# Optimization experiments

Measured on AMD Instinct MI355X. Metric: run time of the kernel, lower is better.

Reference implementation:

```python
import jax, jax.numpy as jnp
import numpy as np

BS, D_IN, D_H, D_Z = 4096, 784, 400, 20


def setup_inputs() -> dict:
    key = jax.random.key(0)
    ks = jax.random.split(key, 13)
    s = 0.05
    return {
        "x": jax.random.normal(ks[0], (BS, D_IN), dtype=jnp.float32),
        "W1": jax.random.normal(ks[1], (D_H, D_IN), dtype=jnp.float32) * s,
        "b1": jax.random.normal(ks[2], (D_H,), dtype=jnp.float32) * s,
        "W21": jax.random.normal(ks[3], (D_Z, D_H), dtype=jnp.float32) * s,
        "b21": jax.random.normal(ks[4], (D_Z,), dtype=jnp.float32) * s,
        "W22": jax.random.normal(ks[5], (D_Z, D_H), dtype=jnp.float32) * s,
        "b22": jax.random.normal(ks[6], (D_Z,), dtype=jnp.float32) * s,
        "W3": jax.random.normal(ks[7], (D_H, D_Z), dtype=jnp.float32) * s,
        "b3": jax.random.normal(ks[8], (D_H,), dtype=jnp.float32) * s,
        "W41": jax.random.normal(ks[9], (D_IN, D_H), dtype=jnp.float32) * s,
        "b41": jax.random.normal(ks[10], (D_IN,), dtype=jnp.float32) * s,
        "W42": jax.random.normal(ks[11], (D_IN, D_H), dtype=jnp.float32) * s,
        "b42": jax.random.normal(ks[12], (D_IN,), dtype=jnp.float32) * s,
    }


def reference(x, W1, b1, W21, b21, W22, b22, W3, b3, W41, b41, W42, b42):
    xr = x.reshape(-1, D_IN)                              # [bs, 784]
    # encode
    h1 = jax.nn.relu(xr @ W1.T + b1)                      # [bs, 400]
    mu = h1 @ W21.T + b21                                 # [bs, 20]
    logvar = h1 @ W22.T + b22                             # [bs, 20]
    # unscented sigma points: varsqrt[:, i] = sqrt(N)*logvar[:, i]*e_i
    N = D_Z
    sqrtN = jnp.asarray(np.sqrt(N), dtype=x.dtype)
    # delta[i, b, j] = sqrt(N) * logvar[b, i] * (i == j)   -> [N, bs, N]
    delta = sqrtN * logvar.T[:, :, None] * jnp.eye(N, dtype=x.dtype)[:, None, :]
    z = jnp.concatenate([mu[None] + delta, mu[None] - delta], axis=0)  # [2N, bs, N]

    def decode(zs):
        h3 = jax.nn.relu(zs @ W3.T + b3)                  # [bs, 400]
        return zs @ W41.T * 0 + (h3 @ W41.T + b41), h3 @ W42.T + b42

    def decode_clean(zs):
        h3 = jax.nn.relu(zs @ W3.T + b3)
        return h3 @ W41.T + b41, h3 @ W42.T + b42

    # original loop decodes every sigma point; recon_x keeps the last one
    mu_x, var_x = jax.vmap(decode_clean)(z)               # each [2N, bs, 784]
    recon_mu = mu_x[-1]
    recon_var = var_x[-1]
    return recon_mu, recon_var, mu, logvar, z
```

## Files before the change

### kernel.cpp

```cpp
#include <hip/hip_runtime.h>
#include <hip/hip_bf16.h>

#define BS   4096
#define DIN  784
#define DH   400
#define DZ   20

#define KPH  416
#define KPD  448

#define OFF_RMU  0
#define OFF_RVAR 3211264
#define OFF_MU   6422528
#define OFF_LV   6504448
#define OFF_Z    6586368

#define WS_WCAT  0
#define WS_W2C   1404928
#define WS_H1B   1444864
#define WS_H3B   4852736

#define SQRT20F 4.47213595499958f

using short8 = __attribute__((ext_vector_type(8))) short;
using f4     = __attribute__((ext_vector_type(4))) float;
using i4     = __attribute__((ext_vector_type(4))) int;

__device__ __forceinline__ short bf16r(float f) {
    union { float f; unsigned u; } v; v.f = f;
    unsigned r = (v.u + 0x7fffu + ((v.u >> 16) & 1u)) >> 16;
    return (short)r;
}

__device__ __forceinline__ i4 pack8(const i4 q0, const i4 q1) {
    i4 d;
    d[0] = (q0[1] & 0xffff0000) | (int)(((unsigned)q0[0]) >> 16);
    d[1] = (q0[3] & 0xffff0000) | (int)(((unsigned)q0[2]) >> 16);
    d[2] = (q1[1] & 0xffff0000) | (int)(((unsigned)q1[0]) >> 16);
    d[3] = (q1[3] & 0xffff0000) | (int)(((unsigned)q1[2]) >> 16);
    return d;
}

__device__ __forceinline__ void glds16(const void* g, void* l) {
    __builtin_amdgcn_global_load_lds(
        (const __attribute__((address_space(1))) unsigned int*)g,
        (__attribute__((address_space(3))) unsigned int*)l,
        16, 0, 0);
}

__global__ __launch_bounds__(256)
void k1(const float* __restrict__ x, const float* __restrict__ W1,
        const float* __restrict__ b1,
        const float* __restrict__ W41, const float* __restrict__ W42,
        const float* __restrict__ W21, const float* __restrict__ W22,
        short* __restrict__ h1b, char* __restrict__ ws) {
    __shared__ short sA[2][64 * 64];
    __shared__ short sB[2][80 * 64];

    const int tid = threadIdx.x;
    const int bid = blockIdx.x;

    if (bid >= 320) {
        short* wcat = (short*)(ws + WS_WCAT);
        short* w2c  = (short*)(ws + WS_W2C);
        const int NC = 1568 * 56 + 48 * 52;
        for (int p = (bid - 320) * 256 + tid; p < NC; p += 64 * 256) {
            const float* sr = nullptr;
            short* dst;
            int c;
            if (p < 1568 * 56) {
                int row = p / 56; c = p - row * 56;
                sr = (row < 784) ? (W41 + (size_t)row * DH)
                                 : (W42 + (size_t)(row - 784) * DH);
                dst = wcat + (size_t)row * KPD + c * 8;
            } else {
                int q = p - 1568 * 56;
                int row = q / 52; c = q - row * 52;
                if (row < 20)      sr = W21 + (size_t)row * DH;
                else if (row < 40) sr = W22 + (size_t)(row - 20) * DH;
                dst = w2c + (size_t)row * KPH + c * 8;
            }
            short8 v;
            if (c < 50 && sr) {
                f4 a = *(const f4*)(sr + c * 8);
                f4 b = *(const f4*)(sr + c * 8 + 4);
#pragma unroll
                for (int e = 0; e < 4; ++e) { v[e] = bf16r(a[e]); v[4 + e] = bf16r(b[e]); }
            } else {
#pragma unroll
                for (int e = 0; e < 8; ++e) v[e] = 0;
            }
            *(short8*)dst = v;
        }
        return;
    }

    const int swz = (bid & 7) * 40 + (bid >> 3);
    const int bm = swz / 5, bn = swz - bm * 5;
    const int w = tid >> 6, l = tid & 63, lg = l >> 4, lr = l & 15;

    f4 acc[5] = {};
    i4 A0[4], A1[4], B0[6], B1[6];

    auto loadT = [&](int kt, i4* qa, i4* qb) {
#pragma unroll
        for (int i = 0; i < 2; ++i) {
            int c = tid + i * 256;
            int row = c >> 3, kc = c & 7;
            int gk = kt * 64 + kc * 8;
            if (gk < DIN) {
                const i4* p = (const i4*)(x + (size_t)(bm * 64 + row) * DIN + gk);
                qa[2 * i] = p[0]; qa[2 * i + 1] = p[1];
            } else {
                qa[2 * i] = (i4){0, 0, 0, 0}; qa[2 * i + 1] = (i4){0, 0, 0, 0};
            }
        }
#pragma unroll
        for (int i = 0; i < 3; ++i) {
            int c = tid + i * 256;
            if (c < 640) {
                int row = c >> 3, kc = c & 7;
                int gk = kt * 64 + kc * 8;
                if (gk < DIN) {
                    const i4* p = (const i4*)(W1 + (size_t)(bn * 80 + row) * DIN + gk);
                    qb[2 * i] = p[0]; qb[2 * i + 1] = p[1];
                } else {
                    qb[2 * i] = (i4){0, 0, 0, 0}; qb[2 * i + 1] = (i4){0, 0, 0, 0};
                }
            }
        }
    };
    auto writeT = [&](int buf, const i4* qa, const i4* qb) {
#pragma unroll
        for (int i = 0; i < 2; ++i) {
            int c = tid + i * 256;
            int row = c >> 3, kc = c & 7;
            *(i4*)&sA[buf][(row * 8 + (kc ^ (row & 7))) * 8] = pack8(qa[2 * i], qa[2 * i + 1]);
        }
#pragma unroll
        for (int i = 0; i < 3; ++i) {
            int c = tid + i * 256;
            if (c < 640) {
                int row = c >> 3, kc = c & 7;
                *(i4*)&sB[buf][(row * 8 + (kc ^ (row & 7))) * 8] = pack8(qb[2 * i], qb[2 * i + 1]);
            }
        }
    };
    auto compute = [&](int buf) {
        const int row = w * 16 + lr;
#pragma unroll
        for (int kk = 0; kk < 2; ++kk) {
            short8 a = *(const short8*)&sA[buf][(row * 8 + ((kk * 4 + lg) ^ (row & 7))) * 8];
#pragma unroll
            for (int ni = 0; ni < 5; ++ni) {
                int brw = ni * 16 + lr;
                short8 b = *(const short8*)&sB[buf][(brw * 8 + ((kk * 4 + lg) ^ (brw & 7))) * 8];
                acc[ni] = __builtin_amdgcn_mfma_f32_16x16x32_bf16(a, b, acc[ni], 0, 0, 0);
            }
        }
    };

    loadT(0, A0, B0);
    writeT(0, A0, B0);
    loadT(1, A1, B1);
    loadT(2, A0, B0);
    asm volatile("s_waitcnt lgkmcnt(0)" ::: "memory");
    __builtin_amdgcn_sched_barrier(0);
    __builtin_amdgcn_s_barrier();
    __builtin_amdgcn_sched_barrier(0);

#pragma unroll
    for (int kt2 = 0; kt2 < 13; kt2 += 2) {
        {
            const int kt = kt2;
            compute(0);
            if (kt <= 11) writeT(1, A1, B1);
            if (kt <= 9)  loadT(kt + 3, A1, B1);
            asm volatile("s_waitcnt lgkmcnt(0)" ::: "memory");
            __builtin_amdgcn_sched_barrier(0);
            __builtin_amdgcn_s_barrier();
            __builtin_amdgcn_sched_barrier(0);
        }
        if (kt2 + 1 < 13) {
            const int kt = kt2 + 1;
            compute(1);
            if (kt <= 11) writeT(0, A0, B0);
            if (kt <= 9)  loadT(kt + 3, A0, B0);
            asm volatile("s_waitcnt lgkmcnt(0)" ::: "memory");
            __builtin_amdgcn_sched_barrier(0);
            __builtin_amdgcn_s_barrier();
            __builtin_amdgcn_sched_barrier(0);
        }
    }

#pragma unroll
    for (int ni = 0; ni < 5; ++ni) {
        int col = bn * 80 + ni * 16 + lr;
        float bias = b1[col];
#pragma unroll
        for (int r = 0; r < 4; ++r) {
            int row = bm * 64 + w * 16 + lg * 4 + r;
            float v = acc[ni][r] + bias;
            h1b[(size_t)row * KPH + col] = bf16r(v > 0.f ? v : 0.f);
        }
    }
    if (bn == 4) {
        for (int p = tid; p < 64 * 16; p += 256) {
            int r = p >> 4, c = 400 + (p & 15);
            h1b[(size_t)(bm * 64 + r) * KPH + c] = 0;
        }
    }
}

__global__ __launch_bounds__(256)
void k_mid(const short* __restrict__ h1b, const short* __restrict__ w2c,
           const float* __restrict__ W3, const float* __restrict__ b3,
           const float* __restrict__ b21, const float* __restrict__ b22,
           float* __restrict__ out, short* __restrict__ h3b) {
    __shared__ short sA[16 * 416];
    __shared__ short sB[48 * 416];
    __shared__ short sW[400 * 40];
    __shared__ float muv[2][16][20];
    __shared__ short zl[16 * 40];
    __shared__ short h3s[16 * 448];

    const int tid = threadIdx.x;
    const int blk = blockIdx.x;
    const int w = tid >> 6, l = tid & 63, lg = l >> 4, lr = l & 15;
    const int r0 = blk * 16;

#pragma unroll
    for (int it = 0; it < 4; ++it) {
        int p = it * 256 + tid;
        if (p < 832) {
            int r = p / 52, cp = p - r * 52, c = cp ^ (r & 3);
            glds16(h1b + (size_t)(r0 + r) * KPH + c * 8, &sA[p * 8]);
        }
    }
#pragma unroll
    for (int it = 0; it < 10; ++it) {
        int p = it * 256 + tid;
        if (p < 2496) {
            int r = p / 52, cp = p - r * 52, c = cp ^ (r & 3);
            glds16(w2c + (size_t)r * KPH + c * 8, &sB[p * 8]);
        }
    }
    if (tid < 200) {
#pragma unroll
        for (int i = 0; i < 2; ++i) {
            int r = tid + i * 200;
            const float* src = W3 + (size_t)r * DZ;
            f4 f0 = *(const f4*)src;
            f4 f1 = *(const f4*)(src + 4);
            f4 f2 = *(const f4*)(src + 8);
            f4 f3 = *(const f4*)(src + 12);
            f4 f5 = *(const f4*)(src + 16);
            short8 c0, c1, c2, c3;
#pragma unroll
            for (int e = 0; e < 4; ++e) {
                c0[e] = bf16r(f0[e]); c0[4 + e] = bf16r(f1[e]);
                c1[e] = bf16r(f2[e]); c1[4 + e] = bf16r(f3[e]);
                c2[e] = bf16r(f5[e]); c2[4 + e] = 0;
                c3[e] = 0; c3[4 + e] = 0;
            }
            *(short8*)&sW[r * 40 + 0]  = c0;
            *(short8*)&sW[r * 40 + 8]  = c1;
            *(short8*)&sW[r * 40 + 16] = c2;
            *(short8*)&sW[r * 40 + 24] = c3;
        }
    }
    __syncthreads();

    if (w == 0) {
        f4 a3[3] = {};
#pragma unroll
        for (int kk = 0; kk < 13; ++kk) {
            short8 a = *(const short8*)&sA[(lr * 52 + ((kk * 4 + lg) ^ (lr & 3))) * 8];
#pragma unroll
            for (int ni = 0; ni < 3; ++ni) {
                int br = ni * 16 + lr;
                short8 b = *(const short8*)&sB[(br * 52 + ((kk * 4 + lg) ^ (br & 3))) * 8];
                a3[ni] = __builtin_amdgcn_mfma_f32_16x16x32_bf16(a, b, a3[ni], 0, 0, 0);
            }
        }
#pragma unroll
        for (int ni = 0; ni < 3; ++ni) {
            int n = ni * 16 + lr;
            if (n < 40) {
                float bias = (n < 20) ? b21[n] : b22[n - 20];
#pragma unroll
                for (int r = 0; r < 4; ++r) {
                    int row = lg * 4 + r;
                    float v = a3[ni][r] + bias;
                    if (n < 20) {
                        muv[0][row][n] = v;
                        out[OFF_MU + (size_t)(r0 + row) * 20 + n] = v;
                    } else {
                        muv[1][row][n - 20] = v;
                        out[OFF_LV + (size_t)(r0 + row) * 20 + (n - 20)] = v;
                    }
                }
            }
        }
    }
    __syncthreads();

    if (tid < 80) {
        int row = tid / 5, c = tid - (tid / 5) * 5;
        short8 v;
#pragma unroll
        for (int e = 0; e < 8; ++e) {
            int j = c * 8 + e;
            float val = 0.f;
            if (j < 20) {
                val = muv[0][row][j];
                if (j == 19) val -= SQRT20F * muv[1][row][19];
            }
            v[e] = bf16r(val);
        }
        *(short8*)&zl[row * 40 + c * 8] = v;
    } else if (tid < 176) {
        int t = tid - 80;
        int row = t / 6, c = t - (t / 6) * 6;
        short8 zz;
#pragma unroll
        for (int e = 0; e < 8; ++e) zz[e] = 0;
        *(short8*)&h3s[row * 448 + 400 + c * 8] = zz;
    }
    __syncthreads();

    for (int f = w; f < 25; f += 4) {
        int n0 = f * 16;
        short8 a = *(const short8*)&zl[lr * 40 + lg * 8];
        short8 b = *(const short8*)&sW[(n0 + lr) * 40 + lg * 8];
        f4 z4 = {};
        f4 accv = __builtin_amdgcn_mfma_f32_16x16x32_bf16(a, b, z4, 0, 0, 0);
        int n = n0 + lr;
        float bias = b3[n];
#pragma unroll
        for (int r = 0; r < 4; ++r) {
            int row = lg * 4 + r;
            float v = accv[r] + bias;
            h3s[row * 448 + n] = bf16r(v > 0.f ? v : 0.f);
        }
    }
    __syncthreads();

#pragma unroll
    for (int it = 0; it < 4; ++it) {
        int p = it * 256 + tid;
        if (p < 896) {
            int row = p / 56, c = p - (p / 56) * 56;
            *(short8*)(h3b + (size_t)(r0 + row) * KPD + c * 8) =
                *(const short8*)&h3s[row * 448 + c * 8];
        }
    }
}

__global__ __launch_bounds__(256)
void k_gemm4(const short* __restrict__ h3b, const short* __restrict__ wcat,
             const float* __restrict__ b41, const float* __restrict__ b42,
             float* __restrict__ out) {
    __shared__ short sA[2][128 * 64];
    __shared__ short sB[2][112 * 64];

    const int tid = threadIdx.x;
    const int bid = blockIdx.x;

    if (bid >= 448) {
        const int zb = bid - 448;
#pragma unroll 2
        for (int it = 0; it < 50; ++it) {
            int idx = it * 16384 + zb * 256 + tid;
            int s = idx / 20480;
            int rem = idx - s * 20480;
            int b = rem / 5, j4 = rem - b * 5;
            int sp = (s < 20) ? s : s - 20;
            f4 v = *(const f4*)(out + OFF_MU + (size_t)b * 20 + j4 * 4);
            if ((sp >> 2) == j4) {
                float add = ((s < 20) ? SQRT20F : -SQRT20F) * out[OFF_LV + (size_t)b * 20 + sp];
                int e = sp & 3;
#pragma unroll
                for (int k = 0; k < 4; ++k) v[k] += (e == k) ? add : 0.f;
            }
            *(f4*)(out + OFF_Z + (size_t)idx * 4) = v;
        }
        return;
    }

    const int swz = (bid & 7) * 56 + (bid >> 3);
    const int bm = swz / 14, bn = swz - bm * 14;
    const int w = tid >> 6, l = tid & 63, lg = l >> 4, lr = l & 15;

    f4 acc[2][7] = {};

    auto stage = [&](int buf, int kt) {
#pragma unroll
        for (int i = 0; i < 4; ++i) {
            int c = tid + i * 256;
            int r = c >> 3, kc = (c & 7) ^ (r & 7);
            glds16(h3b + (size_t)(bm * 128 + r) * KPD + kt * 64 + kc * 8, &sA[buf][c * 8]);
        }
#pragma unroll
        for (int i = 0; i < 4; ++i) {
            int c = tid + i * 256;
            if (c < 896) {
                int r = c >> 3, kc = (c & 7) ^ (r & 7);
                glds16(wcat + (size_t)(bn * 112 + r) * KPD + kt * 64 + kc * 8, &sB[buf][c * 8]);
            }
        }
    };

    stage(0, 0);
    __syncthreads();
    for (int kt = 0; kt < 7; ++kt) {
        const int cur = kt & 1;
        if (kt < 6) stage(cur ^ 1, kt + 1);
        const int row0 = w * 32 + lr, row1 = w * 32 + 16 + lr;
#pragma unroll
        for (int kk = 0; kk < 2; ++kk) {
            short8 a0 = *(const short8*)&sA[cur][(row0 * 8 + ((kk * 4 + lg) ^ (row0 & 7))) * 8];
            short8 a1 = *(const short8*)&sA[cur][(row1 * 8 + ((kk * 4 + lg) ^ (row1 & 7))) * 8];
#pragma unroll
            for (int ni = 0; ni < 7; ++ni) {
                int br = ni * 16 + lr;
                short8 b = *(const short8*)&sB[cur][(br * 8 + ((kk * 4 + lg) ^ (br & 7))) * 8];
                acc[0][ni] = __builtin_amdgcn_mfma_f32_16x16x32_bf16(a0, b, acc[0][ni], 0, 0, 0);
                acc[1][ni] = __builtin_amdgcn_mfma_f32_16x16x32_bf16(a1, b, acc[1][ni], 0, 0, 0);
            }
        }
        __syncthreads();
    }

    const bool first = (bn < 7);
#pragma unroll
    for (int mi = 0; mi < 2; ++mi)
#pragma unroll
        for (int ni = 0; ni < 7; ++ni) {
            int colt = bn * 112 + ni * 16 + lr;
            int cc = first ? colt : colt - 784;
            float bias = first ? b41[cc] : b42[cc];
            size_t base = first ? (size_t)OFF_RMU : (size_t)OFF_RVAR;
#pragma unroll
            for (int r = 0; r < 4; ++r) {
                size_t row = (size_t)(bm * 128 + w * 32 + mi * 16 + lg * 4 + r);
                out[base + row * DIN + cc] = acc[mi][ni][r] + bias;
            }
        }
}

extern "C" void kernel_launch(void* const* d_in, const int* in_sizes, int n_in,
                              void* d_out, int out_size, void* d_ws, size_t ws_size,
                              hipStream_t stream) {
    const float* x   = (const float*)d_in[0];
    const float* W1  = (const float*)d_in[1];
    const float* b1  = (const float*)d_in[2];
    const float* W21 = (const float*)d_in[3];
    const float* b21 = (const float*)d_in[4];
    const float* W22 = (const float*)d_in[5];
    const float* b22 = (const float*)d_in[6];
    const float* W3  = (const float*)d_in[7];
    const float* b3  = (const float*)d_in[8];
    const float* W41 = (const float*)d_in[9];
    const float* b41 = (const float*)d_in[10];
    const float* W42 = (const float*)d_in[11];
    const float* b42 = (const float*)d_in[12];

    float* out = (float*)d_out;
    char*  ws  = (char*)d_ws;
    const short* wcat = (const short*)(ws + WS_WCAT);
    const short* w2c  = (const short*)(ws + WS_W2C);
    short* h1b = (short*)(ws + WS_H1B);
    short* h3b = (short*)(ws + WS_H3B);

    k1<<<384, 256, 0, stream>>>(x, W1, b1, W41, W42, W21, W22, h1b, ws);
    k_mid<<<256, 256, 0, stream>>>(h1b, w2c, W3, b3, b21, b22, out, h3b);
    k_gemm4<<<512, 256, 0, stream>>>(h3b, wcat, b41, b42, out);
}
```

Measured before the change: 49.89 us.

## Pre-convert W1 to bf16 and stage via direct LDS loads; halve gemm4 K-tile

Adds a small kernel that converts W1 to padded bf16 in the workspace, so k1 can stage the B operand with global_load_lds instead of loading fp32 into registers and packing. k1's hand-scheduled triple-register pipeline becomes a simpler double-buffered loop with __syncthreads. k_gemm4's K tile shrinks from 64 to 32, which halves its LDS footprint (likely to raise occupancy) at the cost of twice as many barriers. The extra launch and the simpler k1 pipeline may cost more than they save.

```diff
diff --git a/kernel.cpp b/kernel.cpp
--- a/kernel.cpp
+++ b/kernel.cpp
@@ -6,6 +6,7 @@
 #define DH   400
 #define DZ   20
 
+#define KP1  832
 #define KPH  416
 #define KPD  448
 
@@ -17,8 +18,9 @@
 
 #define WS_WCAT  0
 #define WS_W2C   1404928
-#define WS_H1B   1444864
-#define WS_H3B   4852736
+#define WS_W1B   1444864
+#define WS_H1B   2110464
+#define WS_H3B   5518336
 
 #define SQRT20F 4.47213595499958f
 
@@ -48,9 +50,28 @@
         16, 0, 0);
 }
 
+__global__ void k0(const float* __restrict__ W1, char* __restrict__ ws) {
+    int gid = blockIdx.x * 256 + threadIdx.x;
+    if (gid >= 400 * 104) return;
+    int row = gid / 104, c = gid - row * 104;
+    short* dst = (short*)(ws + WS_W1B) + (size_t)row * KP1 + c * 8;
+    short8 v;
+    if (c < 98) {
+        const float* sr = W1 + (size_t)row * DIN + c * 8;
+        f4 a = *(const f4*)sr;
+        f4 b = *(const f4*)(sr + 4);
+#pragma unroll
+        for (int e = 0; e < 4; ++e) { v[e] = bf16r(a[e]); v[4 + e] = bf16r(b[e]); }
+    } else {
+#pragma unroll
+        for (int e = 0; e < 8; ++e) v[e] = 0;
+    }
+    *(short8*)dst = v;
+}
+
 __global__ __launch_bounds__(256)
-void k1(const float* __restrict__ x, const float* __restrict__ W1,
-        const float* __restrict__ b1,
+void k1(const float* __restrict__ x, const float* __restrict__ b1,
+        const short* __restrict__ W1b,
         const float* __restrict__ W41, const float* __restrict__ W42,
         const float* __restrict__ W21, const float* __restrict__ W22,
         short* __restrict__ h1b, char* __restrict__ ws) {
@@ -100,9 +121,9 @@
     const int w = tid >> 6, l = tid & 63, lg = l >> 4, lr = l & 15;
 
     f4 acc[5] = {};
-    i4 A0[4], A1[4], B0[6], B1[6];
-
-    auto loadT = [&](int kt, i4* qa, i4* qb) {
+    i4 ar[4];
+
+    auto a_load = [&](int kt) {
 #pragma unroll
         for (int i = 0; i < 2; ++i) {
             int c = tid + i * 256;
@@ -110,39 +131,27 @@
             int gk = kt * 64 + kc * 8;
             if (gk < DIN) {
                 const i4* p = (const i4*)(x + (size_t)(bm * 64 + row) * DIN + gk);
-                qa[2 * i] = p[0]; qa[2 * i + 1] = p[1];
+                ar[2 * i] = p[0]; ar[2 * i + 1] = p[1];
             } else {
-                qa[2 * i] = (i4){0, 0, 0, 0}; qa[2 * i + 1] = (i4){0, 0, 0, 0};
-            }
-        }
-#pragma unroll
-        for (int i = 0; i < 3; ++i) {
-            int c = tid + i * 256;
-            if (c < 640) {
-                int row = c >> 3, kc = c & 7;
-                int gk = kt * 64 + kc * 8;
-                if (gk < DIN) {
-                    const i4* p = (const i4*)(W1 + (size_t)(bn * 80 + row) * DIN + gk);
-                    qb[2 * i] = p[0]; qb[2 * i + 1] = p[1];
-                } else {
-                    qb[2 * i] = (i4){0, 0, 0, 0}; qb[2 * i + 1] = (i4){0, 0, 0, 0};
-                }
+                ar[2 * i] = (i4){0, 0, 0, 0}; ar[2 * i + 1] = (i4){0, 0, 0, 0};
             }
         }
     };
-    auto writeT = [&](int buf, const i4* qa, const i4* qb) {
+    auto a_write = [&](int buf) {
 #pragma unroll
         for (int i = 0; i < 2; ++i) {
             int c = tid + i * 256;
             int row = c >> 3, kc = c & 7;
-            *(i4*)&sA[buf][(row * 8 + (kc ^ (row & 7))) * 8] = pack8(qa[2 * i], qa[2 * i + 1]);
-        }
-#pragma unroll
-        for (int i = 0; i < 3; ++i) {
-            int c = tid + i * 256;
-            if (c < 640) {
-                int row = c >> 3, kc = c & 7;
-                *(i4*)&sB[buf][(row * 8 + (kc ^ (row & 7))) * 8] = pack8(qb[2 * i], qb[2 * i + 1]);
+            *(i4*)&sA[buf][(row * 8 + (kc ^ (row & 7))) * 8] = pack8(ar[2 * i], ar[2 * i + 1]);
+        }
+    };
+    auto b_stage = [&](int buf, int kt) {
+#pragma unroll
+        for (int it = 0; it < 3; ++it) {
+            int p = it * 256 + tid;
+            if (p < 640) {
+                int r = p >> 3, kc = (p & 7) ^ (r & 7);
+                glds16(W1b + (size_t)(bn * 80 + r) * KP1 + kt * 64 + kc * 8, &sB[buf][p * 8]);
             }
         }
     };
@@ -160,37 +169,14 @@
         }
     };
 
-    loadT(0, A0, B0);
-    writeT(0, A0, B0);
-    loadT(1, A1, B1);
-    loadT(2, A0, B0);
-    asm volatile("s_waitcnt lgkmcnt(0)" ::: "memory");
-    __builtin_amdgcn_sched_barrier(0);
-    __builtin_amdgcn_s_barrier();
-    __builtin_amdgcn_sched_barrier(0);
-
-#pragma unroll
-    for (int kt2 = 0; kt2 < 13; kt2 += 2) {
-        {
-            const int kt = kt2;
-            compute(0);
-            if (kt <= 11) writeT(1, A1, B1);
-            if (kt <= 9)  loadT(kt + 3, A1, B1);
-            asm volatile("s_waitcnt lgkmcnt(0)" ::: "memory");
-            __builtin_amdgcn_sched_barrier(0);
-            __builtin_amdgcn_s_barrier();
-            __builtin_amdgcn_sched_barrier(0);
-        }
-        if (kt2 + 1 < 13) {
-            const int kt = kt2 + 1;
-            compute(1);
-            if (kt <= 11) writeT(0, A0, B0);
-            if (kt <= 9)  loadT(kt + 3, A0, B0);
-            asm volatile("s_waitcnt lgkmcnt(0)" ::: "memory");
-            __builtin_amdgcn_sched_barrier(0);
-            __builtin_amdgcn_s_barrier();
-            __builtin_amdgcn_sched_barrier(0);
-        }
+    a_load(0); b_stage(0, 0); a_write(0);
+    __syncthreads();
+    for (int kt = 0; kt < 13; ++kt) {
+        const int cur = kt & 1;
+        if (kt < 12) { a_load(kt + 1); b_stage(cur ^ 1, kt + 1); }
+        compute(cur);
+        if (kt < 12) a_write(cur ^ 1);
+        __syncthreads();
     }
 
 #pragma unroll
@@ -361,8 +347,8 @@
 void k_gemm4(const short* __restrict__ h3b, const short* __restrict__ wcat,
              const float* __restrict__ b41, const float* __restrict__ b42,
              float* __restrict__ out) {
-    __shared__ short sA[2][128 * 64];
-    __shared__ short sB[2][112 * 64];
+    __shared__ short sA[2][128 * 32];
+    __shared__ short sB[2][112 * 32];
 
     const int tid = threadIdx.x;
     const int bid = blockIdx.x;
@@ -396,38 +382,35 @@
 
     auto stage = [&](int buf, int kt) {
 #pragma unroll
-        for (int i = 0; i < 4; ++i) {
+        for (int i = 0; i < 2; ++i) {
             int c = tid + i * 256;
-            int r = c >> 3, kc = (c & 7) ^ (r & 7);
-            glds16(h3b + (size_t)(bm * 128 + r) * KPD + kt * 64 + kc * 8, &sA[buf][c * 8]);
-        }
-#pragma unroll
-        for (int i = 0; i < 4; ++i) {
+            int r = c >> 2, kc = (c & 3) ^ (r & 3);
+            glds16(h3b + (size_t)(bm * 128 + r) * KPD + kt * 32 + kc * 8, &sA[buf][c * 8]);
+        }
+#pragma unroll
+        for (int i = 0; i < 2; ++i) {
             int c = tid + i * 256;
-            if (c < 896) {
-                int r = c >> 3, kc = (c & 7) ^ (r & 7);
-                glds16(wcat + (size_t)(bn * 112 + r) * KPD + kt * 64 + kc * 8, &sB[buf][c * 8]);
+            if (c < 448) {
+                int r = c >> 2, kc = (c & 3) ^ (r & 3);
+                glds16(wcat + (size_t)(bn * 112 + r) * KPD + kt * 32 + kc * 8, &sB[buf][c * 8]);
             }
         }
     };
 
     stage(0, 0);
     __syncthreads();
-    for (int kt = 0; kt < 7; ++kt) {
+    for (int kt = 0; kt < 14; ++kt) {
         const int cur = kt & 1;
-        if (kt < 6) stage(cur ^ 1, kt + 1);
+        if (kt < 13) stage(cur ^ 1, kt + 1);
         const int row0 = w * 32 + lr, row1 = w * 32 + 16 + lr;
-#pragma unroll
-        for (int kk = 0; kk < 2; ++kk) {
-            short8 a0 = *(const short8*)&sA[cur][(row0 * 8 + ((kk * 4 + lg) ^ (row0 & 7))) * 8];
-            short8 a1 = *(const short8*)&sA[cur][(row1 * 8 + ((kk * 4 + lg) ^ (row1 & 7))) * 8];
-#pragma unroll
-            for (int ni = 0; ni < 7; ++ni) {
-                int br = ni * 16 + lr;
-                short8 b = *(const short8*)&sB[cur][(br * 8 + ((kk * 4 + lg) ^ (br & 7))) * 8];
-                acc[0][ni] = __builtin_amdgcn_mfma_f32_16x16x32_bf16(a0, b, acc[0][ni], 0, 0, 0);
-                acc[1][ni] = __builtin_amdgcn_mfma_f32_16x16x32_bf16(a1, b, acc[1][ni], 0, 0, 0);
-            }
+        short8 a0 = *(const short8*)&sA[cur][(row0 * 4 + (lg ^ (row0 & 3))) * 8];
+        short8 a1 = *(const short8*)&sA[cur][(row1 * 4 + (lg ^ (row1 & 3))) * 8];
+#pragma unroll
+        for (int ni = 0; ni < 7; ++ni) {
+            int br = ni * 16 + lr;
+            short8 b = *(const short8*)&sB[cur][(br * 4 + (lg ^ (br & 3))) * 8];
+            acc[0][ni] = __builtin_amdgcn_mfma_f32_16x16x32_bf16(a0, b, acc[0][ni], 0, 0, 0);
+            acc[1][ni] = __builtin_amdgcn_mfma_f32_16x16x32_bf16(a1, b, acc[1][ni], 0, 0, 0);
         }
         __syncthreads();
     }
@@ -470,10 +453,12 @@
     char*  ws  = (char*)d_ws;
     const short* wcat = (const short*)(ws + WS_WCAT);
     const short* w2c  = (const short*)(ws + WS_W2C);
+    const short* W1b  = (const short*)(ws + WS_W1B);
     short* h1b = (short*)(ws + WS_H1B);
     short* h3b = (short*)(ws + WS_H3B);
 
-    k1<<<384, 256, 0, stream>>>(x, W1, b1, W41, W42, W21, W22, h1b, ws);
+    k0<<<163, 256, 0, stream>>>(W1, ws);
+    k1<<<384, 256, 0, stream>>>(x, b1, W1b, W41, W42, W21, W22, h1b, ws);
     k_mid<<<256, 256, 0, stream>>>(h1b, w2c, W3, b3, b21, b22, out, h3b);
     k_gemm4<<<512, 256, 0, stream>>>(h3b, wcat, b41, b42, out);
 }
```

Measured after the change: 51.63 us. 3.5% more time.
